# Kernel tuning notes

Hardware: AMD Instinct MI355X
Metric: run time of the kernel (lower is better)

Reference implementation:

```python
import jax, jax.numpy as jnp
import numpy as np

KERNEL = (3, 3)
STRIDE = (1, 1)
# padding='zero', dimPadding='auto' -> pad = ceil((k-1)/2) per side on each dim
PAD = tuple(int(np.ceil((k - 1) / 2)) for k in KERNEL)


def setup_inputs() -> dict:
    key = jax.random.key(0)
    k1, k2 = jax.random.split(key)
    dataset = jax.random.normal(k1, (32, 64, 112, 112), dtype=jnp.float32)
    filters = jax.random.normal(k2, (128, 64, 3, 3), dtype=jnp.float32)
    return {"dataset": dataset, "filters": filters}


def reference(dataset, filters):
    # The torch module's unfold->multiply->sum->fold pipeline computes a plain
    # cross-correlation (conv2d) of NCHW input with OIHW filters, zero padding
    # PAD per side, stride STRIDE. Output: [B, F, Hout, Wout].
    out = jax.lax.conv_general_dilated(
        dataset, filters,
        window_strides=STRIDE,
        padding=((PAD[0], PAD[0]), (PAD[1], PAD[1])),
        dimension_numbers=("NCHW", "OIHW", "NCHW"),
    )
    return out
```

## Files before the change

### kernel.cpp

```cpp
#include <hip/hip_runtime.h>


typedef __attribute__((ext_vector_type(8))) __bf16 bf16x8;
typedef __attribute__((ext_vector_type(4))) float f32x4;
typedef __attribute__((ext_vector_type(4))) unsigned int u32x4;

#define ROWS_PER_KH 124
#define ROW_SHORTS 64

__device__ __forceinline__ unsigned short f2bf(float f) {
    unsigned u = __builtin_bit_cast(unsigned, f);
    u += 0x7FFF + ((u >> 16) & 1);
    return (unsigned short)(u >> 16);
}

__global__ void prep_weights(const float* __restrict__ flt,
                             unsigned short* __restrict__ wsA) {
    int idx = blockIdx.x * 256 + threadIdx.x;
    if (idx >= 9 * 128 * 64) return;
    int off = idx >> 13;
    int f   = (idx >> 6) & 127;
    int c   = idx & 63;
    wsA[idx] = f2bf(flt[(f * 64 + c) * 9 + off]);
}

__global__ __launch_bounds__(512, 4)
void conv_mfma(const float* __restrict__ x,
               const unsigned short* __restrict__ wsA,
               float* __restrict__ out) {
    __shared__ __align__(16) unsigned short Bs[4 * ROWS_PER_KH * ROW_SHORTS];

    const int tid = threadIdx.x;
    const int id  = blockIdx.x;
    const int xcd = id & 7;
    const int s   = id >> 3;
    const int b   = s / 7;
    const int hpl = s - b * 7;
    const int hp  = xcd * 7 + hpl;
    const int h0  = hp * 2;

    if (tid < 32) {
        int kh = tid >> 3, cq = tid & 7;
        int R = kh * ROWS_PER_KH;
        int chunk = cq ^ (R & 7);
        *(u32x4*)&Bs[R * ROW_SHORTS + chunk * 8] = u32x4{0, 0, 0, 0};
    }

    const int li   = tid & 7;
    const int unit = tid >> 3;
    for (int it = 0; it < 8; ++it) {
        int u = it * 64 + unit;
        if (u < 480) {
            int wo = u >> 5;
            int rc = u & 31;
            int rp = rc >> 3;
            int cq = rc & 7;
            int hr = h0 + rp - 1;
            int c  = cq * 8 + li;
            f32x4 f0 = {0.f, 0.f, 0.f, 0.f}, f1 = {0.f, 0.f, 0.f, 0.f};
            if ((unsigned)hr < 112u && wo < 14) {
                const float* src = x + (((size_t)b * 64 + c) * 112 + hr) * 112 + wo * 8;
                f0 = *(const f32x4*)src;
                f1 = *(const f32x4*)(src + 4);
            }
            float r[8] = {f0.x, f0.y, f0.z, f0.w, f1.x, f1.y, f1.z, f1.w};
#pragma unroll
            for (int d = 1; d < 8; d <<= 1) {
#pragma unroll
                for (int jA = 0; jA < 8; ++jA) {
                    if (jA & d) continue;
                    int jB = jA | d;
                    float give = (li & d) ? r[jA] : r[jB];
                    float got  = __shfl_xor(give, d, 64);
                    if (li & d) r[jA] = got; else r[jB] = got;
                }
            }
            int R = rp * ROWS_PER_KH + wo * 8 + li + 1;
            int chunk = cq ^ (R & 7);
            unsigned pk[4];
#pragma unroll
            for (int j = 0; j < 4; ++j)
                pk[j] = (unsigned)f2bf(r[2 * j]) | ((unsigned)f2bf(r[2 * j + 1]) << 16);
            *(u32x4*)&Bs[R * ROW_SHORTS + chunk * 8] = u32x4{pk[0], pk[1], pk[2], pk[3]};
        }
    }
    __syncthreads();

    const int lane = tid & 63;
    const int wid  = tid >> 6;
    const int fg   = wid & 3;
    const int rr   = wid >> 2;
    const int q    = lane >> 4;
    const int l16  = lane & 15;
    const int h    = h0 + rr;

    f32x4 acc[2][7];
#pragma unroll
    for (int mt = 0; mt < 2; ++mt)
#pragma unroll
        for (int tw = 0; tw < 7; ++tw)
            acc[mt][tw] = {0.f, 0.f, 0.f, 0.f};

    const unsigned short* wA = wsA + (fg * 32 + l16) * 64 + q * 8;

#pragma unroll
    for (int off = 0; off < 9; ++off) {
        const int kh = off / 3;
        const int kw = off - kh * 3;
        const int Rbase = (rr + kh) * ROWS_PER_KH + kw;
#pragma unroll
        for (int cs = 0; cs < 2; ++cs) {
            bf16x8 a0 = *(const bf16x8*)(wA + off * 8192 + cs * 32);
            bf16x8 a1 = *(const bf16x8*)(wA + off * 8192 + 1024 + cs * 32);
            const int cq = cs * 4 + q;
#pragma unroll
            for (int tw = 0; tw < 7; ++tw) {
                int R = Rbase + tw * 16 + l16;
                int chunk = cq ^ (R & 7);
                bf16x8 bv = *(const bf16x8*)&Bs[R * ROW_SHORTS + chunk * 8];
                acc[0][tw] = __builtin_amdgcn_mfma_f32_16x16x32_bf16(a0, bv, acc[0][tw], 0, 0, 0);
                acc[1][tw] = __builtin_amdgcn_mfma_f32_16x16x32_bf16(a1, bv, acc[1][tw], 0, 0, 0);
            }
        }
    }

#pragma unroll
    for (int mt = 0; mt < 2; ++mt) {
#pragma unroll
        for (int tw = 0; tw < 7; ++tw) {
            int f = fg * 32 + mt * 16 + q * 4;
            int w = tw * 16 + l16;
            float* o = out + (((size_t)b * 128 + f) * 112 + h) * 112 + w;
#pragma unroll
            for (int r2 = 0; r2 < 4; ++r2)
                o[(size_t)r2 * 12544] = acc[mt][tw][r2];
        }
    }
}

extern "C" void kernel_launch(void* const* d_in, const int* in_sizes, int n_in,
                              void* d_out, int out_size, void* d_ws, size_t ws_size,
                              hipStream_t stream) {
    const float* x   = (const float*)d_in[0];
    const float* flt = (const float*)d_in[1];
    float* out = (float*)d_out;
    unsigned short* wsA = (unsigned short*)d_ws;

    hipLaunchKernelGGL(prep_weights, dim3(288), dim3(256), 0, stream, flt, wsA);
    hipLaunchKernelGGL(conv_mfma, dim3(1792), dim3(512), 0, stream, x, wsA, out);
}
```

Measured before the change: 350.5 us.

## Pre-transpose input to padded bf16 NHWC and load tiles via global_load_lds

Adds a prep_input kernel that converts the fp32 NCHW input into a zero-padded bf16 channel-last, swizzled buffer in workspace. The conv kernel then fills shared memory with direct global-to-LDS loads instead of per-block transpose and convert work. Each wave now covers 64 filters (4 M-tiles) over part of the width, rather than 32 filters over the full width. This removes redundant halo conversion and shuffle work per block, but adds an extra pass over the input in global memory and an extra kernel launch. The old path is kept as a fallback when the workspace is too small.

```diff
diff --git a/kernel.cpp b/kernel.cpp
--- a/kernel.cpp
+++ b/kernel.cpp
@@ -5,13 +5,19 @@
 typedef __attribute__((ext_vector_type(4))) float f32x4;
 typedef __attribute__((ext_vector_type(4))) unsigned int u32x4;
 
-#define ROWS_PER_KH 124
-#define ROW_SHORTS 64
+#define XROW 7296
+#define WPROW 120
 
 __device__ __forceinline__ unsigned short f2bf(float f) {
     unsigned u = __builtin_bit_cast(unsigned, f);
     u += 0x7FFF + ((u >> 16) & 1);
     return (unsigned short)(u >> 16);
+}
+
+__device__ __forceinline__ void gload_lds16(const unsigned short* g, unsigned short* l) {
+    __builtin_amdgcn_global_load_lds(
+        (const __attribute__((address_space(1))) unsigned int*)g,
+        (__attribute__((address_space(3))) unsigned int*)l, 16, 0, 0);
 }
 
 __global__ void prep_weights(const float* __restrict__ flt,
@@ -25,10 +31,160 @@
 }
 
 __global__ __launch_bounds__(512, 4)
+void prep_input(const float* __restrict__ x, unsigned short* __restrict__ xt) {
+    __shared__ __align__(16) unsigned short T[112 * 64];
+    const int tid  = threadIdx.x;
+    const int b    = blockIdx.x / 112;
+    const int h    = blockIdx.x - b * 112;
+    const int li   = tid & 7;
+    const int unit = tid >> 3;
+
+    for (int it = 0; it < 2; ++it) {
+        int u = it * 64 + unit;
+        if (u < 112) {
+            int wo = u >> 3, cq = u & 7;
+            int c  = cq * 8 + li;
+            const float* src = x + (((size_t)b * 64 + c) * 112 + h) * 112 + wo * 8;
+            f32x4 f0 = *(const f32x4*)src;
+            f32x4 f1 = *(const f32x4*)(src + 4);
+            float r[8] = {f0.x, f0.y, f0.z, f0.w, f1.x, f1.y, f1.z, f1.w};
+#pragma unroll
+            for (int d = 1; d < 8; d <<= 1) {
+#pragma unroll
+                for (int jA = 0; jA < 8; ++jA) {
+                    if (jA & d) continue;
+                    int jB = jA | d;
+                    float give = (li & d) ? r[jA] : r[jB];
+                    float got  = __shfl_xor(give, d, 64);
+                    if (li & d) r[jA] = got; else r[jB] = got;
+                }
+            }
+            unsigned pk[4];
+#pragma unroll
+            for (int j = 0; j < 4; ++j)
+                pk[j] = (unsigned)f2bf(r[2 * j]) | ((unsigned)f2bf(r[2 * j + 1]) << 16);
+            int w = wo * 8 + li;
+            *(u32x4*)&T[w * 64 + (cq ^ (w & 7)) * 8] = u32x4{pk[0], pk[1], pk[2], pk[3]};
+        }
+    }
+    __syncthreads();
+
+    unsigned short* dst = xt + ((size_t)b * 114 + (h + 1)) * XROW;
+    for (int ch = tid; ch < 912; ch += 512) {
+        int wp = ch >> 3, cq = ch & 7;
+        u32x4 v = {0, 0, 0, 0};
+        if (wp >= 1 && wp <= 112) {
+            int w = wp - 1;
+            v = *(const u32x4*)&T[w * 64 + (cq ^ (w & 7)) * 8];
+        }
+        *(u32x4*)&dst[(size_t)ch * 8] = v;
+    }
+    if (h == 0 || h == 111) {
+        unsigned short* zr = xt + ((size_t)b * 114 + (h == 0 ? 0 : 113)) * XROW;
+        for (int ch = tid; ch < 912; ch += 512)
+            *(u32x4*)&zr[(size_t)ch * 8] = u32x4{0, 0, 0, 0};
+    }
+}
+
+template <int TW0, int NTW>
+__device__ __forceinline__ void wave_kloop(const unsigned short* Bs,
+                                           const unsigned short* wA,
+                                           float* obase, int rr, int l16, int q) {
+    f32x4 acc[4][NTW];
+#pragma unroll
+    for (int mt = 0; mt < 4; ++mt)
+#pragma unroll
+        for (int t = 0; t < NTW; ++t) acc[mt][t] = {0.f, 0.f, 0.f, 0.f};
+
+#pragma unroll
+    for (int off = 0; off < 9; ++off) {
+        const int kh = off / 3;
+        const int kw = off - kh * 3;
+        const int rp = rr + kh;
+#pragma unroll
+        for (int cs = 0; cs < 2; ++cs) {
+            bf16x8 a0 = *(const bf16x8*)(wA + off * 8192 + cs * 32);
+            bf16x8 a1 = *(const bf16x8*)(wA + off * 8192 + 1024 + cs * 32);
+            bf16x8 a2 = *(const bf16x8*)(wA + off * 8192 + 2048 + cs * 32);
+            bf16x8 a3 = *(const bf16x8*)(wA + off * 8192 + 3072 + cs * 32);
+            const int cq = cs * 4 + q;
+#pragma unroll
+            for (int t = 0; t < NTW; ++t) {
+                int wp = (TW0 + t) * 16 + l16 + kw;
+                int chunk = cq ^ (wp & 7);
+                bf16x8 bv = *(const bf16x8*)&Bs[(rp * WPROW + wp) * 64 + chunk * 8];
+                acc[0][t] = __builtin_amdgcn_mfma_f32_16x16x32_bf16(a0, bv, acc[0][t], 0, 0, 0);
+                acc[1][t] = __builtin_amdgcn_mfma_f32_16x16x32_bf16(a1, bv, acc[1][t], 0, 0, 0);
+                acc[2][t] = __builtin_amdgcn_mfma_f32_16x16x32_bf16(a2, bv, acc[2][t], 0, 0, 0);
+                acc[3][t] = __builtin_amdgcn_mfma_f32_16x16x32_bf16(a3, bv, acc[3][t], 0, 0, 0);
+            }
+        }
+    }
+#pragma unroll
+    for (int mt = 0; mt < 4; ++mt)
+#pragma unroll
+        for (int t = 0; t < NTW; ++t) {
+            float* o = obase + (size_t)(mt * 16) * 12544 + (TW0 + t) * 16 + l16;
+#pragma unroll
+            for (int r2 = 0; r2 < 4; ++r2)
+                o[(size_t)r2 * 12544] = acc[mt][t][r2];
+        }
+}
+
+__global__ __launch_bounds__(512, 4)
+void conv_fast(const unsigned short* __restrict__ xt,
+               const unsigned short* __restrict__ wsA,
+               float* __restrict__ out) {
+    __shared__ __align__(16) unsigned short Bs[4 * WPROW * 64];
+
+    const int tid = threadIdx.x;
+    const int id  = blockIdx.x;
+    const int xcd = id & 7;
+    const int s   = id >> 3;
+    const int b   = s / 7;
+    const int hpl = s - b * 7;
+    const int h0  = (xcd * 7 + hpl) * 2;
+
+    const int lane = tid & 63;
+    const int wid  = tid >> 6;
+
+    {
+        const unsigned short* xbase = xt + ((size_t)b * 114 + h0) * XROW;
+        const int l3 = lane >> 3, j = lane & 7;
+        for (int i = wid; i < 60; i += 8) {
+            int rp  = i / 15;
+            int seg = i - rp * 15;
+            int wp  = seg * 8 + l3;
+            int wps = wp <= 113 ? wp : 113;
+            const unsigned short* src =
+                xbase + (size_t)rp * XROW + wps * 64 + ((j ^ (wps & 7)) * 8);
+            gload_lds16(src, &Bs[(rp * WPROW + seg * 8) * 64]);
+        }
+    }
+    __syncthreads();
+
+    const int l16 = lane & 15;
+    const int q   = lane >> 4;
+    const int fg  = wid & 1;
+    const int rr  = (wid >> 1) & 1;
+    const int ws  = wid >> 2;
+    const int h   = h0 + rr;
+
+    const unsigned short* wA = wsA + (fg * 64 + l16) * 64 + q * 8;
+    float* obase = out + (((size_t)b * 128 + fg * 64 + q * 4) * 112 + h) * 112;
+
+    if (ws == 0) wave_kloop<0, 4>(Bs, wA, obase, rr, l16, q);
+    else         wave_kloop<4, 3>(Bs, wA, obase, rr, l16, q);
+}
+
+#define ROWS_PER_KH 124
+#define ROW_SHORTS 64
+
+__global__ __launch_bounds__(512, 4)
 void conv_mfma(const float* __restrict__ x,
                const unsigned short* __restrict__ wsA,
                float* __restrict__ out) {
-    __shared__ __align__(16) unsigned short Bs[4 * ROWS_PER_KH * ROW_SHORTS];
+    __shared__ __align__(16) unsigned short Bso[4 * ROWS_PER_KH * ROW_SHORTS];
 
     const int tid = threadIdx.x;
     const int id  = blockIdx.x;
@@ -43,7 +199,7 @@
         int kh = tid >> 3, cq = tid & 7;
         int R = kh * ROWS_PER_KH;
         int chunk = cq ^ (R & 7);
-        *(u32x4*)&Bs[R * ROW_SHORTS + chunk * 8] = u32x4{0, 0, 0, 0};
+        *(u32x4*)&Bso[R * ROW_SHORTS + chunk * 8] = u32x4{0, 0, 0, 0};
     }
 
     const int li   = tid & 7;
@@ -81,7 +237,7 @@
 #pragma unroll
             for (int j = 0; j < 4; ++j)
                 pk[j] = (unsigned)f2bf(r[2 * j]) | ((unsigned)f2bf(r[2 * j + 1]) << 16);
-            *(u32x4*)&Bs[R * ROW_SHORTS + chunk * 8] = u32x4{pk[0], pk[1], pk[2], pk[3]};
+            *(u32x4*)&Bso[R * ROW_SHORTS + chunk * 8] = u32x4{pk[0], pk[1], pk[2], pk[3]};
         }
     }
     __syncthreads();
@@ -117,7 +273,7 @@
             for (int tw = 0; tw < 7; ++tw) {
                 int R = Rbase + tw * 16 + l16;
                 int chunk = cq ^ (R & 7);
-                bf16x8 bv = *(const bf16x8*)&Bs[R * ROW_SHORTS + chunk * 8];
+                bf16x8 bv = *(const bf16x8*)&Bso[R * ROW_SHORTS + chunk * 8];
                 acc[0][tw] = __builtin_amdgcn_mfma_f32_16x16x32_bf16(a0, bv, acc[0][tw], 0, 0, 0);
                 acc[1][tw] = __builtin_amdgcn_mfma_f32_16x16x32_bf16(a1, bv, acc[1][tw], 0, 0, 0);
             }
@@ -147,5 +303,14 @@
     unsigned short* wsA = (unsigned short*)d_ws;
 
     hipLaunchKernelGGL(prep_weights, dim3(288), dim3(256), 0, stream, flt, wsA);
-    hipLaunchKernelGGL(conv_mfma, dim3(1792), dim3(512), 0, stream, x, wsA, out);
-}
+
+    const size_t XT_BYTES = (size_t)32 * 114 * 114 * 64 * 2;
+    const size_t need = 147456 + XT_BYTES;
+    if (ws_size >= need) {
+        unsigned short* xxt = wsA + 147456 / 2;
+        hipLaunchKernelGGL(prep_input, dim3(3584), dim3(512), 0, stream, x, xxt);
+        hipLaunchKernelGGL(conv_fast, dim3(1792), dim3(512), 0, stream, xxt, wsA, out);
+    } else {
+        hipLaunchKernelGGL(conv_mfma, dim3(1792), dim3(512), 0, stream, x, wsA, out);
+    }
+}
```

Measured after the change: 406.1 us. 1.16x slower.
